# Optimization experiments

Hardware: AMD Instinct MI355X
Metric: run time of the kernel (lower is better)

## Reference

```python
import jax, jax.numpy as jnp
import numpy as np
from jax import lax

HIDDEN_CH = 32
KS = 3


def _conv(x, w):
    # x: [B, Cin, H, W], w: [Cout, Cin, k, k] -> [B, Cout, H, W] (SAME padding)
    return lax.conv_general_dilated(
        x, w, window_strides=(1, 1), padding='SAME',
        dimension_numbers=('NCHW', 'OIHW', 'NCHW'))


def _cell(x, h, gw, gb, cw, cb):
    combined = jnp.concatenate([x, h], axis=1)
    gates = jax.nn.sigmoid(_conv(combined, gw) + gb[None, :, None, None])
    r, z = jnp.split(gates, 2, axis=1)
    combined_r = jnp.concatenate([x, r * h], axis=1)
    n = jnp.tanh(_conv(combined_r, cw) + cb[None, :, None, None])
    return (1.0 - z) * h + z * n


def setup_inputs() -> dict:
    key = jax.random.key(0)
    ks = jax.random.split(key, 9)
    B, T, H, W = 8, 16, 128, 128
    hc = HIDDEN_CH
    seq = jax.random.normal(ks[0], (B, T, H, W), dtype=jnp.float32)

    def conv_init(k, cout, cin):
        fan_in = cin * KS * KS
        bound = 1.0 / np.sqrt(fan_in)
        return jax.random.uniform(k, (cout, cin, KS, KS), jnp.float32, -bound, bound)

    def bias_init(k, cout, cin):
        bound = 1.0 / np.sqrt(cin * KS * KS)
        return jax.random.uniform(k, (cout,), jnp.float32, -bound, bound)

    # Layer 0: input_ch=1, layer 1: input_ch=hc
    gw0 = conv_init(ks[1], 2 * hc, 1 + hc)
    gb0 = bias_init(ks[2], 2 * hc, 1 + hc)
    cw0 = conv_init(ks[3], hc, 1 + hc)
    cb0 = bias_init(ks[4], hc, 1 + hc)
    gw1 = conv_init(ks[5], 2 * hc, hc + hc)
    gb1 = bias_init(ks[6], 2 * hc, hc + hc)
    cw1 = conv_init(ks[7], hc, hc + hc)
    cb1 = bias_init(ks[8], hc, hc + hc)
    return {'seq': seq, 'gw0': gw0, 'gb0': gb0, 'cw0': cw0, 'cb0': cb0,
            'gw1': gw1, 'gb1': gb1, 'cw1': cw1, 'cb1': cb1}


def reference(seq, gw0, gb0, cw0, cb0, gw1, gb1, cw1, cb1):
    B, T, H, W = seq.shape
    hc = HIDDEN_CH
    h0 = jnp.zeros((B, hc, H, W), dtype=seq.dtype)
    h1 = jnp.zeros((B, hc, H, W), dtype=seq.dtype)
    # xs: [T, B, 1, H, W]
    xs = jnp.transpose(seq, (1, 0, 2, 3))[:, :, None, :, :]

    def step(carry, x_t):
        h0, h1 = carry
        h0 = _cell(x_t, h0, gw0, gb0, cw0, cb0)
        h1 = _cell(h0, h1, gw1, gb1, cw1, cb1)
        return (h0, h1), None

    (h0, h1), _ = lax.scan(step, (h0, h1), xs)
    return h1
```

## Files before the change

kernel.cpp:

```cpp
#include <hip/hip_runtime.h>


#define HH 128
#define PH 130
#define HW 16384
#define BB 8
#define TT 16

typedef _Float16 f16x8 __attribute__((ext_vector_type(8)));
typedef float f32x4 __attribute__((ext_vector_type(4)));
typedef unsigned int u32x4 __attribute__((ext_vector_type(4)));

__device__ __forceinline__ unsigned short f2h(float x){
    return __builtin_bit_cast(unsigned short, (_Float16)x);
}
__device__ __forceinline__ float h2f(unsigned short u){
    return (float)__builtin_bit_cast(_Float16, u);
}
__device__ __forceinline__ f16x8 ld_frag(const unsigned short* p){
    u32x4 v = *(const u32x4*)p;
    return __builtin_bit_cast(f16x8, v);
}
__device__ __forceinline__ f16x8 lds_frag_w(const unsigned short* base, int spix, int q){
    u32x4 v = *(const u32x4*)(base + spix * 32 + q * 8);
    return __builtin_bit_cast(f16x8, v);
}
__device__ __forceinline__ float sigmoid_f(float a){ return 1.0f / (1.0f + __expf(-a)); }
__device__ __forceinline__ float tanh_f(float a){ float e2 = __expf(2.0f * a); return 1.0f - 2.0f / (e2 + 1.0f); }
__device__ __forceinline__ unsigned int packh2(float lo, float hi){
    return (unsigned int)f2h(lo) | ((unsigned int)f2h(hi) << 16);
}

struct SmemT {
    unsigned short hs[2][13824];
    unsigned short rh[10880];
    float xt[444];
};

__device__ __forceinline__ void halo_rc10(int s, int& gr, int& gc){
    s = s > 83 ? 83 : s;
    if (s < 34)      { gr = 0;            gc = s;      }
    else if (s < 68) { gr = 9;            gc = s - 34; }
    else if (s < 76) { gr = 1 + (s - 68); gc = 0;      }
    else             { gr = 1 + (s - 76); gc = 33;     }
}

__device__ __forceinline__ f16x8 x_im2col(const float* xt, int gr, int gc, int q){
    f16x8 v;
#pragma unroll
    for (int j = 0; j < 8; ++j) {
        int k = q * 8 + j;
        float f = 0.0f;
        if (k < 9) f = xt[(gr + k / 3) * 37 + gc + k % 3];
        v[j] = (_Float16)f;
    }
    return v;
}

__device__ __forceinline__ void stage_chunk(unsigned short* slot,
    const unsigned short* __restrict__ g, int b, int pr0, int pc0, int k, int lane)
{
    int chunk = k * 64 + lane;
    int pix = chunk >> 2, part = chunk & 3;
    int r = pix / 36, c = pix - r * 36;
    int pr = pr0 + r; pr = pr < 0 ? 0 : (pr > 129 ? 129 : pr);
    int pc = pc0 + c; pc = pc < 0 ? 0 : (pc > 129 ? 129 : pc);
    const unsigned short* ga = g + ((long)((b * PH + pr) * PH + pc) * 32 + part * 8);
    __builtin_amdgcn_global_load_lds(
        (const __attribute__((address_space(1))) unsigned int*)ga,
        (__attribute__((address_space(3))) unsigned int*)(slot + k * 512),
        16, 0, 0);
}

__device__ __forceinline__ void stage_plane12(unsigned short* slot,
    const unsigned short* __restrict__ g, int b, int pr0, int pc0)
{
    const int wv = threadIdx.x >> 6, lane = threadIdx.x & 63;
    for (int k = wv; k < 27; k += 8)
        stage_chunk(slot, g, b, pr0, pc0, k, lane);
}

__device__ __forceinline__ void stage_x12(float* xt, const float* __restrict__ seq,
                                          int b, int t, int R0, int C0)
{
    if (threadIdx.x < 444) {
        int p = threadIdx.x;
        int r = p / 37, c = p - r * 37;
        int ir = R0 - 2 + r, ic = C0 - 2 + c;
        float v = 0.0f;
        if (ir >= 0 && ir < HH && ic >= 0 && ic < HH)
            v = seq[((long)b * TT + t) * HW + ir * HH + ic];
        xt[p] = v;
    }
}

__global__ void prep_w(const float* __restrict__ w, unsigned short* __restrict__ wf,
                       int CO, int CIT, int NSTEP, int xmode)
{
    int idx = blockIdx.x * 256 + threadIdx.x;
    int total = NSTEP * CO * 32;
    if (idx >= total) return;
    int kk = idx & 31;
    int t  = idx >> 5;
    int co = t % CO;
    int s  = t / CO;
    int lco = (co & ~31) | (2 * (co & 15) + ((co >> 4) & 1));
    float v = 0.0f;
    if (xmode && s == NSTEP - 1) {
        if (kk < 9) v = w[(lco * CIT + 0) * 9 + kk];
    } else {
        int tap = s % 9;
        int cin = (s / 9) * 32 + kk + (xmode ? 1 : 0);
        v = w[(lco * CIT + cin) * 9 + tap];
    }
    wf[idx] = f2h(v);
}

template<int L, int EMIT, int SPLIT>
__device__ __forceinline__ void cell_compute(SmemT& sm,
    const unsigned short* __restrict__ hs1src,
    unsigned short* __restrict__ Hout,
    const unsigned short* __restrict__ Wg, const float* __restrict__ bg,
    const unsigned short* __restrict__ Wc, const float* __restrict__ bc,
    float* __restrict__ out, int b, int R0, int C0)
{
    constexpr int KG = (L == 0) ? 10 : 18;
    constexpr int KC = (L == 0) ? 10 : 18;

    const int wv = threadIdx.x >> 6, lane = threadIdx.x & 63;
    const int m16 = lane & 15, q = lane >> 4;
    const unsigned short* hp = (L == 0) ? sm.hs[0] : sm.hs[1];

    f16x8 Bc[4];
#pragma unroll
    for (int ng = 0; ng < 4; ++ng)
        Bc[ng] = ld_frag(Wg + (ng * 16 + m16) * 32 + q * 8);
    f16x8 Cc[2];
#pragma unroll
    for (int ng = 0; ng < 2; ++ng)
        Cc[ng] = ld_frag(Wc + (ng * 16 + m16) * 32 + q * 8);

    __syncthreads();

    const bool HASH = (wv >= 2);
    int hgr = 0, hgc = 0;
    halo_rc10((wv - 2) * 16 + m16, hgr, hgc);

    f32x4 gI[2][4];
    f32x4 gH[2];
#pragma unroll
    for (int ng = 0; ng < 4; ++ng) {
        float bv = bg[(ng >> 1) * 32 + 2 * m16 + (ng & 1)];
#pragma unroll
        for (int mg = 0; mg < 2; ++mg) gI[mg][ng] = f32x4{bv, bv, bv, bv};
        if (ng < 2) gH[ng] = f32x4{bv, bv, bv, bv};
    }

#pragma unroll
    for (int s = 0; s < KG; ++s) {
        if (SPLIT && s == 9) __syncthreads();
        f16x8 Bn[4];
        if (s + 1 < KG) {
#pragma unroll
            for (int ng = 0; ng < 4; ++ng)
                Bn[ng] = ld_frag(Wg + ((s + 1) * 64 + ng * 16 + m16) * 32 + q * 8);
        }
        if (SPLIT && s < 4) {
            int k = wv + 8 * s;
            if (k < 27)
                stage_chunk(sm.hs[1], hs1src, b, R0 - 1, C0 - 1, k, lane);
        }
        f16x8 AI[2], AH;
        if (L == 0 && s == 9) {
#pragma unroll
            for (int mg = 0; mg < 2; ++mg)
                AI[mg] = x_im2col(sm.xt, wv + 1, mg * 16 + 1 + m16, q);
            AH = x_im2col(sm.xt, hgr, hgc, q);
        } else {
            const int tap = (L == 0) ? s : (s % 9);
            const unsigned short* pl = (L == 1 && s >= 9) ? sm.hs[1] : sm.hs[0];
#pragma unroll
            for (int mg = 0; mg < 2; ++mg)
                AI[mg] = lds_frag_w(pl, (wv + 1 + tap / 3) * 36 + mg * 16 + 1 + m16 + tap % 3, q);
            AH = lds_frag_w(pl, (hgr + tap / 3) * 36 + hgc + tap % 3, q);
        }
#pragma unroll
        for (int mg = 0; mg < 2; ++mg)
#pragma unroll
            for (int ng = 0; ng < 4; ++ng)
                gI[mg][ng] = __builtin_amdgcn_mfma_f32_16x16x32_f16(AI[mg], Bc[ng], gI[mg][ng], 0, 0, 0);
        if (HASH) {
#pragma unroll
            for (int ng = 0; ng < 2; ++ng)
                gH[ng] = __builtin_amdgcn_mfma_f32_16x16x32_f16(AH, Bc[ng], gH[ng], 0, 0, 0);
        }
        if (s + 1 < KG) {
#pragma unroll
            for (int ng = 0; ng < 4; ++ng) Bc[ng] = Bn[ng];
        }
    }

    unsigned int zpk[2][4];
#pragma unroll
    for (int mg = 0; mg < 2; ++mg)
#pragma unroll
        for (int rg = 0; rg < 4; ++rg) {
            int gr = wv + 1, gc = mg * 16 + 1 + q * 4 + rg;
            zpk[mg][rg] = packh2(sigmoid_f(gI[mg][2][rg]), sigmoid_f(gI[mg][3][rg]));
            float rv0 = sigmoid_f(gI[mg][0][rg]);
            float rv1 = sigmoid_f(gI[mg][1][rg]);
            unsigned int hvp = *(const unsigned int*)(hp + ((gr + 1) * 36 + gc + 1) * 32 + 2 * m16);
            float h0 = h2f((unsigned short)hvp), h1 = h2f((unsigned short)(hvp >> 16));
            *(unsigned int*)(sm.rh + (gr * 34 + gc) * 32 + 2 * m16) = packh2(rv0 * h0, rv1 * h1);
        }
    if (HASH) {
#pragma unroll
        for (int rg = 0; rg < 4; ++rg) {
            int gr, gc; halo_rc10((wv - 2) * 16 + q * 4 + rg, gr, gc);
            float rv0 = sigmoid_f(gH[0][rg]);
            float rv1 = sigmoid_f(gH[1][rg]);
            unsigned int hvp = *(const unsigned int*)(hp + ((gr + 1) * 36 + gc + 1) * 32 + 2 * m16);
            float h0 = h2f((unsigned short)hvp), h1 = h2f((unsigned short)(hvp >> 16));
            *(unsigned int*)(sm.rh + (gr * 34 + gc) * 32 + 2 * m16) = packh2(rv0 * h0, rv1 * h1);
        }
    }
    __syncthreads();

    f32x4 cacc[2][2];
#pragma unroll
    for (int mg = 0; mg < 2; ++mg)
#pragma unroll
        for (int ng = 0; ng < 2; ++ng) {
            float bv = bc[2 * m16 + ng];
            cacc[mg][ng] = f32x4{bv, bv, bv, bv};
        }
#pragma unroll
    for (int s = 0; s < KC; ++s) {
        f16x8 Cn[2];
        if (s + 1 < KC) {
#pragma unroll
            for (int ng = 0; ng < 2; ++ng)
                Cn[ng] = ld_frag(Wc + ((s + 1) * 32 + ng * 16 + m16) * 32 + q * 8);
        }
        f16x8 A2[2];
        if (L == 0 && s == 9) {
#pragma unroll
            for (int mg = 0; mg < 2; ++mg)
                A2[mg] = x_im2col(sm.xt, wv + 1, mg * 16 + 1 + m16, q);
        } else if (L == 1 && s < 9) {
#pragma unroll
            for (int mg = 0; mg < 2; ++mg)
                A2[mg] = lds_frag_w(sm.hs[0], (wv + 1 + s / 3) * 36 + mg * 16 + m16 + 1 + s % 3, q);
        } else {
            const int tap = (L == 0) ? s : (s - 9);
#pragma unroll
            for (int mg = 0; mg < 2; ++mg)
                A2[mg] = lds_frag_w(sm.rh, (wv + tap / 3) * 34 + mg * 16 + m16 + tap % 3, q);
        }
#pragma unroll
        for (int mg = 0; mg < 2; ++mg)
#pragma unroll
            for (int ng = 0; ng < 2; ++ng)
                cacc[mg][ng] = __builtin_amdgcn_mfma_f32_16x16x32_f16(A2[mg], Cc[ng], cacc[mg][ng], 0, 0, 0);
        if (s + 1 < KC) {
#pragma unroll
            for (int ng = 0; ng < 2; ++ng) Cc[ng] = Cn[ng];
        }
    }

    unsigned int hvout[2][4];
#pragma unroll
    for (int mg = 0; mg < 2; ++mg)
#pragma unroll
        for (int rg = 0; rg < 4; ++rg) {
            int lcol = mg * 16 + q * 4 + rg;
            float nv0 = tanh_f(cacc[mg][0][rg]);
            float nv1 = tanh_f(cacc[mg][1][rg]);
            float zz0 = h2f((unsigned short)zpk[mg][rg]);
            float zz1 = h2f((unsigned short)(zpk[mg][rg] >> 16));
            unsigned int hop = *(const unsigned int*)(hp + ((wv + 2) * 36 + lcol + 2) * 32 + 2 * m16);
            float ho0 = h2f((unsigned short)hop), ho1 = h2f((unsigned short)(hop >> 16));
            float hn0 = (1.0f - zz0) * ho0 + zz0 * nv0;
            float hn1 = (1.0f - zz1) * ho1 + zz1 * nv1;
            if (!EMIT) {
                long psp = (long)(b * PH + R0 + wv + 1) * PH + (C0 + lcol + 1);
                *(unsigned int*)(Hout + psp * 32 + 2 * m16) = packh2(hn0, hn1);
            } else {
                hvout[mg][rg] = packh2(hn0, hn1);
            }
        }

    if (EMIT) {
        __syncthreads();
        unsigned short* scr = sm.rh;
#pragma unroll
        for (int mg = 0; mg < 2; ++mg)
#pragma unroll
            for (int rg = 0; rg < 4; ++rg)
                *(unsigned int*)(scr + ((wv * 32 + mg * 16 + q * 4 + rg) * 32) + 2 * m16)
                    = hvout[mg][rg];
        __syncthreads();
        const int tid = threadIdx.x;
        const int rowid = tid >> 1, half = tid & 1;
        const int n = rowid >> 3, wr = rowid & 7;
        long obase = ((long)(b * 32 + n) * HH + (R0 + wr)) * HH + C0 + half * 16;
#pragma unroll
        for (int j = 0; j < 16; ++j)
            out[obase + j] = h2f(scr[(wr * 32 + half * 16 + j) * 32 + n]);
    }
}

__global__ __launch_bounds__(512, 4)
void cell_l0(const unsigned short* __restrict__ Hin, unsigned short* __restrict__ Hout,
             const float* __restrict__ seq, int t,
             const unsigned short* __restrict__ Wg, const float* __restrict__ bg,
             const unsigned short* __restrict__ Wc, const float* __restrict__ bc)
{
    __shared__ __align__(16) SmemT sm;
    const int wg = blockIdx.x;
    const int b = wg >> 6, tr = (wg >> 2) & 15, tc = wg & 3;
    const int R0 = tr * 8, C0 = tc * 32;
    stage_x12(sm.xt, seq, b, t, R0, C0);
    stage_plane12(sm.hs[0], Hin, b, R0 - 1, C0 - 1);
    cell_compute<0, 0, 0>(sm, (const unsigned short*)0, Hout,
                          Wg, bg, Wc, bc, (float*)0, b, R0, C0);
}

__global__ __launch_bounds__(512, 4)
void step_pair(const unsigned short* __restrict__ h1r, unsigned short* __restrict__ h1w,
               const unsigned short* __restrict__ h0r, unsigned short* __restrict__ h0w,
               const float* __restrict__ seq, int tnext,
               const unsigned short* __restrict__ WG0, const float* __restrict__ gb0,
               const unsigned short* __restrict__ WC0, const float* __restrict__ cb0,
               const unsigned short* __restrict__ WG1, const float* __restrict__ gb1,
               const unsigned short* __restrict__ WC1, const float* __restrict__ cb1)
{
    __shared__ __align__(16) SmemT sm;
    const int wg = blockIdx.x;
    const int b = wg >> 6, tr = (wg >> 2) & 15, tc = wg & 3;
    const int R0 = tr * 8, C0 = tc * 32;
    if (blockIdx.z == 0) {
        stage_plane12(sm.hs[0], h0r, b, R0 - 1, C0 - 1);
        cell_compute<1, 0, 1>(sm, h1r, h1w,
                              WG1, gb1, WC1, cb1, (float*)0, b, R0, C0);
    } else {
        stage_x12(sm.xt, seq, b, tnext, R0, C0);
        stage_plane12(sm.hs[0], h0r, b, R0 - 1, C0 - 1);
        cell_compute<0, 0, 0>(sm, (const unsigned short*)0, h0w,
                              WG0, gb0, WC0, cb0, (float*)0, b, R0, C0);
    }
}

__global__ __launch_bounds__(512, 4)
void cell_l1_emit(const unsigned short* __restrict__ Hin,
                  const unsigned short* __restrict__ Xin,
                  const unsigned short* __restrict__ Wg, const float* __restrict__ bg,
                  const unsigned short* __restrict__ Wc, const float* __restrict__ bc,
                  float* __restrict__ out)
{
    __shared__ __align__(16) SmemT sm;
    const int wg = blockIdx.x;
    const int b = wg >> 6, tr = (wg >> 2) & 15, tc = wg & 3;
    const int R0 = tr * 8, C0 = tc * 32;
    stage_plane12(sm.hs[0], Xin, b, R0 - 1, C0 - 1);
    cell_compute<1, 1, 1>(sm, Hin, (unsigned short*)0,
                          Wg, bg, Wc, bc, out, b, R0, C0);
}

extern "C" void kernel_launch(void* const* d_in, const int* in_sizes, int n_in,
                              void* d_out, int out_size, void* d_ws, size_t ws_size,
                              hipStream_t stream)
{
    const float* seq = (const float*)d_in[0];
    const float* gw0 = (const float*)d_in[1];
    const float* gb0 = (const float*)d_in[2];
    const float* cw0 = (const float*)d_in[3];
    const float* cb0 = (const float*)d_in[4];
    const float* gw1 = (const float*)d_in[5];
    const float* gb1 = (const float*)d_in[6];
    const float* cw1 = (const float*)d_in[7];
    const float* cb1 = (const float*)d_in[8];
    float* out = (float*)d_out;

    const size_t NSP = (size_t)BB * PH * PH * 32;

    char* p = (char*)d_ws;
    unsigned short* S0A = (unsigned short*)p; p += NSP * 2;
    unsigned short* S0B = (unsigned short*)p; p += NSP * 2;
    unsigned short* S1A = (unsigned short*)p; p += NSP * 2;
    unsigned short* S1B = (unsigned short*)p; p += NSP * 2;
    unsigned short* WG0 = (unsigned short*)p; p += 20480 * 2;
    unsigned short* WC0 = (unsigned short*)p; p += 10240 * 2;
    unsigned short* WG1 = (unsigned short*)p; p += 36864 * 2;
    unsigned short* WC1 = (unsigned short*)p; p += 18432 * 2;

    hipMemsetAsync(S0A, 0, 4 * NSP * 2, stream);

    prep_w<<<(10 * 64 * 32 + 255) / 256, 256, 0, stream>>>(gw0, WG0, 64, 33, 10, 1);
    prep_w<<<(10 * 32 * 32 + 255) / 256, 256, 0, stream>>>(cw0, WC0, 32, 33, 10, 1);
    prep_w<<<(18 * 64 * 32 + 255) / 256, 256, 0, stream>>>(gw1, WG1, 64, 64, 18, 0);
    prep_w<<<(18 * 32 * 32 + 255) / 256, 256, 0, stream>>>(cw1, WC1, 32, 64, 18, 0);

    dim3 grid1(512, 1, 1), grid2(512, 1, 2), block(512);

    cell_l0<<<grid1, block, 0, stream>>>(S0A, S0B, seq, 0, WG0, gb0, WC0, cb0);

    unsigned short *h0r = S0B, *h0w = S0A, *h1r = S1A, *h1w = S1B;
    for (int t = 0; t < TT - 1; ++t) {
        step_pair<<<grid2, block, 0, stream>>>(h1r, h1w, h0r, h0w, seq, t + 1,
                                               WG0, gb0, WC0, cb0,
                                               WG1, gb1, WC1, cb1);
        unsigned short* tmp;
        tmp = h0r; h0r = h0w; h0w = tmp;
        tmp = h1r; h1r = h1w; h1w = tmp;
    }
    cell_l1_emit<<<grid1, block, 0, stream>>>(h1r, h0r, WG1, gb1, WC1, cb1, out);
}
```

Before: 974.6 us.

## Shrink LDS footprint by aliasing r*h into h planes and staging 11 rows

The separate r*h buffer is removed. r*h values are kept in registers, a barrier is added, and they are then written over the consumed hidden-state plane, so shared memory drops from three buffers to two. Only 11 of the 12 halo rows are staged. The rare last-row halo fragments are loaded directly from global memory, and the old h values are reused from registers for the final blend. Launch bounds are raised from 4 to 6 blocks per CU to use the smaller LDS for occupancy. The cost is an extra barrier, more live registers, and scattered global loads for the missing row.

```diff
diff --git a/kernel.cpp b/kernel.cpp
--- a/kernel.cpp
+++ b/kernel.cpp
@@ -25,6 +25,12 @@
     u32x4 v = *(const u32x4*)(base + spix * 32 + q * 8);
     return __builtin_bit_cast(f16x8, v);
 }
+__device__ __forceinline__ f16x8 gfragc(const unsigned short* __restrict__ g,
+                                        int b, int pr, int pc, int q){
+    pr = pr < 0 ? 0 : (pr > PH - 1 ? PH - 1 : pr);
+    pc = pc < 0 ? 0 : (pc > PH - 1 ? PH - 1 : pc);
+    return ld_frag(g + (long)((b * PH + pr) * PH + pc) * 32 + q * 8);
+}
 __device__ __forceinline__ float sigmoid_f(float a){ return 1.0f / (1.0f + __expf(-a)); }
 __device__ __forceinline__ float tanh_f(float a){ float e2 = __expf(2.0f * a); return 1.0f - 2.0f / (e2 + 1.0f); }
 __device__ __forceinline__ unsigned int packh2(float lo, float hi){
@@ -32,8 +38,8 @@
 }
 
 struct SmemT {
-    unsigned short hs[2][13824];
-    unsigned short rh[10880];
+    unsigned short r1[12800];
+    unsigned short r2[12800];
     float xt[444];
 };
 
@@ -61,6 +67,7 @@
     const unsigned short* __restrict__ g, int b, int pr0, int pc0, int k, int lane)
 {
     int chunk = k * 64 + lane;
+    chunk = chunk > 1583 ? 1583 : chunk;
     int pix = chunk >> 2, part = chunk & 3;
     int r = pix / 36, c = pix - r * 36;
     int pr = pr0 + r; pr = pr < 0 ? 0 : (pr > 129 ? 129 : pr);
@@ -72,11 +79,11 @@
         16, 0, 0);
 }
 
-__device__ __forceinline__ void stage_plane12(unsigned short* slot,
+__device__ __forceinline__ void stage_plane11(unsigned short* slot,
     const unsigned short* __restrict__ g, int b, int pr0, int pc0)
 {
     const int wv = threadIdx.x >> 6, lane = threadIdx.x & 63;
-    for (int k = wv; k < 27; k += 8)
+    for (int k = wv; k < 25; k += 8)
         stage_chunk(slot, g, b, pr0, pc0, k, lane);
 }
 
@@ -118,7 +125,8 @@
 
 template<int L, int EMIT, int SPLIT>
 __device__ __forceinline__ void cell_compute(SmemT& sm,
-    const unsigned short* __restrict__ hs1src,
+    const unsigned short* __restrict__ g0,
+    const unsigned short* __restrict__ g1,
     unsigned short* __restrict__ Hout,
     const unsigned short* __restrict__ Wg, const float* __restrict__ bg,
     const unsigned short* __restrict__ Wc, const float* __restrict__ bc,
@@ -129,7 +137,8 @@
 
     const int wv = threadIdx.x >> 6, lane = threadIdx.x & 63;
     const int m16 = lane & 15, q = lane >> 4;
-    const unsigned short* hp = (L == 0) ? sm.hs[0] : sm.hs[1];
+    const unsigned short* hp = (L == 0) ? sm.r1 : sm.r2;
+    unsigned short* rhb = (L == 0) ? sm.r1 : sm.r2;
 
     f16x8 Bc[4];
 #pragma unroll
@@ -167,8 +176,8 @@
         }
         if (SPLIT && s < 4) {
             int k = wv + 8 * s;
-            if (k < 27)
-                stage_chunk(sm.hs[1], hs1src, b, R0 - 1, C0 - 1, k, lane);
+            if (k < 25)
+                stage_chunk(sm.r2, g1, b, R0 - 1, C0 - 1, k, lane);
         }
         f16x8 AI[2], AH;
         if (L == 0 && s == 9) {
@@ -178,11 +187,14 @@
             AH = x_im2col(sm.xt, hgr, hgc, q);
         } else {
             const int tap = (L == 0) ? s : (s % 9);
-            const unsigned short* pl = (L == 1 && s >= 9) ? sm.hs[1] : sm.hs[0];
+            const unsigned short* pl  = (L == 1 && s >= 9) ? sm.r2 : sm.r1;
+            const unsigned short* gpl = (L == 1 && s >= 9) ? g1 : g0;
 #pragma unroll
             for (int mg = 0; mg < 2; ++mg)
                 AI[mg] = lds_frag_w(pl, (wv + 1 + tap / 3) * 36 + mg * 16 + 1 + m16 + tap % 3, q);
-            AH = lds_frag_w(pl, (hgr + tap / 3) * 36 + hgc + tap % 3, q);
+            int hr = hgr + tap / 3, hc = hgc + tap % 3;
+            if (hr <= 10) AH = lds_frag_w(pl, hr * 36 + hc, q);
+            else          AH = gfragc(gpl, b, R0 - 1 + hr, C0 - 1 + hc, q);
         }
 #pragma unroll
         for (int mg = 0; mg < 2; ++mg)
@@ -200,7 +212,7 @@
         }
     }
 
-    unsigned int zpk[2][4];
+    unsigned int zpk[2][4], hvp_i[2][4], rhw_i[2][4], rhw_h[4];
 #pragma unroll
     for (int mg = 0; mg < 2; ++mg)
 #pragma unroll
@@ -210,8 +222,9 @@
             float rv0 = sigmoid_f(gI[mg][0][rg]);
             float rv1 = sigmoid_f(gI[mg][1][rg]);
             unsigned int hvp = *(const unsigned int*)(hp + ((gr + 1) * 36 + gc + 1) * 32 + 2 * m16);
+            hvp_i[mg][rg] = hvp;
             float h0 = h2f((unsigned short)hvp), h1 = h2f((unsigned short)(hvp >> 16));
-            *(unsigned int*)(sm.rh + (gr * 34 + gc) * 32 + 2 * m16) = packh2(rv0 * h0, rv1 * h1);
+            rhw_i[mg][rg] = packh2(rv0 * h0, rv1 * h1);
         }
     if (HASH) {
 #pragma unroll
@@ -221,7 +234,22 @@
             float rv1 = sigmoid_f(gH[1][rg]);
             unsigned int hvp = *(const unsigned int*)(hp + ((gr + 1) * 36 + gc + 1) * 32 + 2 * m16);
             float h0 = h2f((unsigned short)hvp), h1 = h2f((unsigned short)(hvp >> 16));
-            *(unsigned int*)(sm.rh + (gr * 34 + gc) * 32 + 2 * m16) = packh2(rv0 * h0, rv1 * h1);
+            rhw_h[rg] = packh2(rv0 * h0, rv1 * h1);
+        }
+    }
+    __syncthreads();
+#pragma unroll
+    for (int mg = 0; mg < 2; ++mg)
+#pragma unroll
+        for (int rg = 0; rg < 4; ++rg) {
+            int gr = wv + 1, gc = mg * 16 + 1 + q * 4 + rg;
+            *(unsigned int*)(rhb + (gr * 34 + gc) * 32 + 2 * m16) = rhw_i[mg][rg];
+        }
+    if (HASH) {
+#pragma unroll
+        for (int rg = 0; rg < 4; ++rg) {
+            int gr, gc; halo_rc10((wv - 2) * 16 + q * 4 + rg, gr, gc);
+            *(unsigned int*)(rhb + (gr * 34 + gc) * 32 + 2 * m16) = rhw_h[rg];
         }
     }
     __syncthreads();
@@ -250,12 +278,12 @@
         } else if (L == 1 && s < 9) {
 #pragma unroll
             for (int mg = 0; mg < 2; ++mg)
-                A2[mg] = lds_frag_w(sm.hs[0], (wv + 1 + s / 3) * 36 + mg * 16 + m16 + 1 + s % 3, q);
+                A2[mg] = lds_frag_w(sm.r1, (wv + 1 + s / 3) * 36 + mg * 16 + m16 + 1 + s % 3, q);
         } else {
             const int tap = (L == 0) ? s : (s - 9);
 #pragma unroll
             for (int mg = 0; mg < 2; ++mg)
-                A2[mg] = lds_frag_w(sm.rh, (wv + tap / 3) * 34 + mg * 16 + m16 + tap % 3, q);
+                A2[mg] = lds_frag_w(rhb, (wv + tap / 3) * 34 + mg * 16 + m16 + tap % 3, q);
         }
 #pragma unroll
         for (int mg = 0; mg < 2; ++mg)
@@ -278,7 +306,7 @@
             float nv1 = tanh_f(cacc[mg][1][rg]);
             float zz0 = h2f((unsigned short)zpk[mg][rg]);
             float zz1 = h2f((unsigned short)(zpk[mg][rg] >> 16));
-            unsigned int hop = *(const unsigned int*)(hp + ((wv + 2) * 36 + lcol + 2) * 32 + 2 * m16);
+            unsigned int hop = hvp_i[mg][rg];
             float ho0 = h2f((unsigned short)hop), ho1 = h2f((unsigned short)(hop >> 16));
             float hn0 = (1.0f - zz0) * ho0 + zz0 * nv0;
             float hn1 = (1.0f - zz1) * ho1 + zz1 * nv1;
@@ -292,7 +320,7 @@
 
     if (EMIT) {
         __syncthreads();
-        unsigned short* scr = sm.rh;
+        unsigned short* scr = sm.r2;
 #pragma unroll
         for (int mg = 0; mg < 2; ++mg)
 #pragma unroll
@@ -310,7 +338,7 @@
     }
 }
 
-__global__ __launch_bounds__(512, 4)
+__global__ __launch_bounds__(512, 6)
 void cell_l0(const unsigned short* __restrict__ Hin, unsigned short* __restrict__ Hout,
              const float* __restrict__ seq, int t,
              const unsigned short* __restrict__ Wg, const float* __restrict__ bg,
@@ -321,12 +349,12 @@
     const int b = wg >> 6, tr = (wg >> 2) & 15, tc = wg & 3;
     const int R0 = tr * 8, C0 = tc * 32;
     stage_x12(sm.xt, seq, b, t, R0, C0);
-    stage_plane12(sm.hs[0], Hin, b, R0 - 1, C0 - 1);
-    cell_compute<0, 0, 0>(sm, (const unsigned short*)0, Hout,
+    stage_plane11(sm.r1, Hin, b, R0 - 1, C0 - 1);
+    cell_compute<0, 0, 0>(sm, Hin, Hin, Hout,
                           Wg, bg, Wc, bc, (float*)0, b, R0, C0);
 }
 
-__global__ __launch_bounds__(512, 4)
+__global__ __launch_bounds__(512, 6)
 void step_pair(const unsigned short* __restrict__ h1r, unsigned short* __restrict__ h1w,
                const unsigned short* __restrict__ h0r, unsigned short* __restrict__ h0w,
                const float* __restrict__ seq, int tnext,
@@ -340,18 +368,18 @@
     const int b = wg >> 6, tr = (wg >> 2) & 15, tc = wg & 3;
     const int R0 = tr * 8, C0 = tc * 32;
     if (blockIdx.z == 0) {
-        stage_plane12(sm.hs[0], h0r, b, R0 - 1, C0 - 1);
-        cell_compute<1, 0, 1>(sm, h1r, h1w,
+        stage_plane11(sm.r1, h0r, b, R0 - 1, C0 - 1);
+        cell_compute<1, 0, 1>(sm, h0r, h1r, h1w,
                               WG1, gb1, WC1, cb1, (float*)0, b, R0, C0);
     } else {
         stage_x12(sm.xt, seq, b, tnext, R0, C0);
-        stage_plane12(sm.hs[0], h0r, b, R0 - 1, C0 - 1);
-        cell_compute<0, 0, 0>(sm, (const unsigned short*)0, h0w,
+        stage_plane11(sm.r1, h0r, b, R0 - 1, C0 - 1);
+        cell_compute<0, 0, 0>(sm, h0r, h0r, h0w,
                               WG0, gb0, WC0, cb0, (float*)0, b, R0, C0);
     }
 }
 
-__global__ __launch_bounds__(512, 4)
+__global__ __launch_bounds__(512, 6)
 void cell_l1_emit(const unsigned short* __restrict__ Hin,
                   const unsigned short* __restrict__ Xin,
                   const unsigned short* __restrict__ Wg, const float* __restrict__ bg,
@@ -362,8 +390,8 @@
     const int wg = blockIdx.x;
     const int b = wg >> 6, tr = (wg >> 2) & 15, tc = wg & 3;
     const int R0 = tr * 8, C0 = tc * 32;
-    stage_plane12(sm.hs[0], Xin, b, R0 - 1, C0 - 1);
-    cell_compute<1, 1, 1>(sm, Hin, (unsigned short*)0,
+    stage_plane11(sm.r1, Xin, b, R0 - 1, C0 - 1);
+    cell_compute<1, 1, 1>(sm, Xin, Hin, (unsigned short*)0,
                           Wg, bg, Wc, bc, out, b, R0, C0);
 }
 
```

New measurement: 3.054 ms. 3.13x slower.
